# Performance work log

Measured on AMD Instinct MI355X. Metric: run time of the kernel, lower is better.

The kernel has to match this reference:

```python
import jax, jax.numpy as jnp
import numpy as np

ALPHA, BETA, GAMMA = 2.0, 2.0, 1.0
EPS = 1e-8  # torch F.cosine_similarity eps
B, T, D = 64, 1024, 256


def setup_inputs() -> dict:
    key = jax.random.key(0)
    k1, k2, k3 = jax.random.split(key, 3)
    f_v = jax.random.normal(k1, (B, T, D), dtype=jnp.float32)
    f_a = jax.random.normal(k2, (B, T, D), dtype=jnp.float32)
    labels = jax.random.randint(k3, (B,), 0, 2, dtype=jnp.int64)
    return {"f_v": f_v, "f_a": f_a, "labels": labels}


def _normalize(x):
    n = jnp.sqrt(jnp.sum(x * x, axis=-1, keepdims=True))
    return x / jnp.maximum(n, EPS)


def reference(f_v, f_a, labels):
    b, t, _ = f_v.shape
    vn = _normalize(f_v)  # [B,T,D]
    an = _normalize(f_a)  # [B,T,D]

    # --- per-timestep aligned-pair term ---
    cos_bt = jnp.sum(vn * an, axis=-1)  # [B,T] cosine sim
    d_bt = 1.0 - cos_bt                  # cosine distance
    pos_mask = (labels == 0).astype(f_v.dtype)[:, None]  # [B,1]
    neg_mask = 1.0 - pos_mask
    loss_pos = ALPHA * jnp.sum(d_bt * pos_mask)
    cnt_pos = jnp.sum(pos_mask) * t
    loss_neg = BETA * jnp.sum((1.0 - d_bt) * neg_mask)  # (1-d) == cos
    cnt_neg = jnp.sum(neg_mask) * t

    # --- cross-sample term: for i != j, (1 - mean_t d_ij) = mean_t cos(v_i_t, a_j_t) ---
    cross_cos = jnp.einsum('itd,jtd->ij', vn, an) / t  # [B,B] mean over T
    offdiag = 1.0 - jnp.eye(b, dtype=f_v.dtype)
    loss_neg = loss_neg + GAMMA * jnp.sum(cross_cos * offdiag)
    cnt_neg = cnt_neg + b * (b - 1)

    loss = jnp.where(cnt_pos > 0, loss_pos / jnp.maximum(cnt_pos, 1.0), 0.0)
    loss = loss + jnp.where(cnt_neg > 0, loss_neg / jnp.maximum(cnt_neg, 1.0), 0.0)
    return loss
```

## Files before the change

### kernel.cpp

```cpp
#include <hip/hip_runtime.h>

constexpr int Bn = 64;
constexpr int Tn = 1024;
constexpr int Dn = 256;

constexpr int TPB   = 256;
constexpr int RG    = 16;
constexpr int NG    = Bn / RG;
constexpr int PITCH = Dn + 4;

__device__ __forceinline__ float dot4(const float4& a, const float4& b) {
    return a.x * b.x + a.y * b.y + a.z * b.z + a.w * b.w;
}

__global__ __launch_bounds__(TPB, 4)
void cmfm_main(const float* __restrict__ fv, const float* __restrict__ fa,
               const int* __restrict__ labels, float* __restrict__ acc) {
    __shared__ __align__(16) float Vs[RG][PITCH];
    __shared__ __align__(16) float As[RG][PITCH];
    __shared__ float rvl[RG];
    __shared__ float ral[RG];
    __shared__ float wred[4][TPB / 64];

    const int tid = threadIdx.x;
    const int r16 = tid >> 4;
    const int dp  = tid & 15;
    const int t   = blockIdx.x;

    const float4* __restrict__ fv4 = reinterpret_cast<const float4*>(fv);
    const float4* __restrict__ fa4 = reinterpret_cast<const float4*>(fa);

    float pos_acc = 0.f, neg_acc = 0.f, diag_acc = 0.f;
    float svd = 0.f, sad = 0.f;

    for (int g = 0; g < NG; ++g) {
        const int row = g * RG + r16;
        const size_t base = ((size_t)row * Tn + t) * (Dn / 4);

        float4 v4[4], a4[4];
        #pragma unroll
        for (int k = 0; k < 4; ++k) {
            v4[k] = fv4[base + dp + 16 * k];
            a4[k] = fa4[base + dp + 16 * k];
        }
        float sqv = 0.f, sqa = 0.f, dva = 0.f;
        #pragma unroll
        for (int k = 0; k < 4; ++k) {
            sqv += dot4(v4[k], v4[k]);
            sqa += dot4(a4[k], a4[k]);
            dva += dot4(v4[k], a4[k]);
            const int d = (dp + 16 * k) * 4;
            *reinterpret_cast<float4*>(&Vs[r16][d]) = v4[k];
            *reinterpret_cast<float4*>(&As[r16][d]) = a4[k];
        }
        #pragma unroll
        for (int off = 1; off < 16; off <<= 1) {
            sqv += __shfl_xor(sqv, off);
            sqa += __shfl_xor(sqa, off);
            dva += __shfl_xor(dva, off);
        }
        if (dp == 0) {
            const float rv = 1.f / fmaxf(sqrtf(sqv), 1e-8f);
            const float ra = 1.f / fmaxf(sqrtf(sqa), 1e-8f);
            rvl[r16] = rv;
            ral[r16] = ra;
            const float cosd = dva * rv * ra;
            diag_acc += cosd;
            if (labels[row] == 0) pos_acc += 1.f - cosd;
            else                  neg_acc += cosd;
        }
        __syncthreads();

        #pragma unroll
        for (int i = 0; i < RG; ++i) {
            svd = fmaf(rvl[i], Vs[i][tid], svd);
            sad = fmaf(ral[i], As[i][tid], sad);
        }
        __syncthreads();
    }

    float dotp = svd * sad;
    #pragma unroll
    for (int off = 1; off < 64; off <<= 1) {
        pos_acc  += __shfl_xor(pos_acc, off);
        neg_acc  += __shfl_xor(neg_acc, off);
        diag_acc += __shfl_xor(diag_acc, off);
        dotp     += __shfl_xor(dotp, off);
    }
    const int wave = tid >> 6;
    const int lane = tid & 63;
    if (lane == 0) {
        wred[0][wave] = pos_acc;
        wred[1][wave] = neg_acc;
        wred[2][wave] = dotp;
        wred[3][wave] = diag_acc;
    }
    __syncthreads();
    if (tid == 0) {
        float p = 0.f, n = 0.f, o = 0.f, dg = 0.f;
        #pragma unroll
        for (int w = 0; w < TPB / 64; ++w) {
            p += wred[0][w]; n += wred[1][w]; o += wred[2][w]; dg += wred[3][w];
        }
        atomicAdd(&acc[0], p);
        atomicAdd(&acc[1], n);
        atomicAdd(&acc[2], o);
        atomicAdd(&acc[3], dg);
    }
}

__global__ void cmfm_final(const int* __restrict__ labels, const float* __restrict__ acc,
                           float* __restrict__ out) {
    if (threadIdx.x == 0) {
        int npos = 0;
        for (int i = 0; i < Bn; ++i) npos += (labels[i] == 0);
        const float pos_sum  = acc[0];
        const float neg_sum  = acc[1];
        const float dot_sum  = acc[2];
        const float diag_sum = acc[3];
        const float cross_sum = dot_sum - diag_sum;

        const float cnt_pos = (float)npos * (float)Tn;
        const float cnt_neg = (float)(Bn - npos) * (float)Tn + (float)Bn * (float)(Bn - 1);

        float loss = 0.f;
        if (npos > 0) loss += 2.0f * pos_sum / cnt_pos;
        loss += (2.0f * neg_sum + 1.0f * cross_sum / (float)Tn) / cnt_neg;
        out[0] = loss;
    }
}

extern "C" void kernel_launch(void* const* d_in, const int* in_sizes, int n_in,
                              void* d_out, int out_size, void* d_ws, size_t ws_size,
                              hipStream_t stream) {
    const float* fv     = (const float*)d_in[0];
    const float* fa     = (const float*)d_in[1];
    const int*   labels = (const int*)d_in[2];
    float* acc = (float*)d_ws;
    float* out = (float*)d_out;

    hipMemsetAsync(acc, 0, 4 * sizeof(float), stream);
    cmfm_main<<<Tn, TPB, 0, stream>>>(fv, fa, labels, acc);
    cmfm_final<<<1, 64, 0, stream>>>(labels, acc, out);
}
```

Measured before the change: 187.5 us.

## Split fused kernel into norms pass and cross-sum pass with workspace scales

The single fused kernel is split into two kernels. The first computes per-(sample, timestep) inverse norms and the diagonal cosine terms with many small blocks and writes the scales to workspace. The second rereads both inputs and accumulates the norm-scaled sums across samples, with no per-group syncthreads loop. This removes the serialized load/sync/LDS rounds and raises parallelism, at the cost of reading the 128 MB of input twice and adding a kernel launch.

```diff
diff --git a/kernel.cpp b/kernel.cpp
--- a/kernel.cpp
+++ b/kernel.cpp
@@ -1,112 +1,129 @@
 #include <hip/hip_runtime.h>
 
-constexpr int Bn = 64;
-constexpr int Tn = 1024;
-constexpr int Dn = 256;
-
-constexpr int TPB   = 256;
-constexpr int RG    = 16;
-constexpr int NG    = Bn / RG;
-constexpr int PITCH = Dn + 4;
+constexpr int Bn  = 64;
+constexpr int Tn  = 1024;
+constexpr int Dn  = 256;
+constexpr int TPB = 256;
 
 __device__ __forceinline__ float dot4(const float4& a, const float4& b) {
     return a.x * b.x + a.y * b.y + a.z * b.z + a.w * b.w;
 }
 
-__global__ __launch_bounds__(TPB, 4)
-void cmfm_main(const float* __restrict__ fv, const float* __restrict__ fa,
-               const int* __restrict__ labels, float* __restrict__ acc) {
-    __shared__ __align__(16) float Vs[RG][PITCH];
-    __shared__ __align__(16) float As[RG][PITCH];
-    __shared__ float rvl[RG];
-    __shared__ float ral[RG];
-    __shared__ float wred[4][TPB / 64];
+__global__ __launch_bounds__(TPB)
+void cmfm_norms(const float* __restrict__ fv, const float* __restrict__ fa,
+                const int* __restrict__ labels,
+                float* __restrict__ rv_ws, float* __restrict__ ra_ws,
+                float* __restrict__ acc) {
+    __shared__ float wred[3][4];
+    const int tid  = threadIdx.x;
+    const int lane = tid & 63;
+    const int wv   = tid >> 6;
+    const int i    = blockIdx.x >> 5;
+    const int tb   = blockIdx.x & 31;
+    const int tt   = lane >> 3;
+    const int d8   = lane & 7;
+    const int t    = tb * 32 + wv * 8 + tt;
 
-    const int tid = threadIdx.x;
-    const int r16 = tid >> 4;
-    const int dp  = tid & 15;
-    const int t   = blockIdx.x;
+    const float4* __restrict__ fv4 = reinterpret_cast<const float4*>(fv);
+    const float4* __restrict__ fa4 = reinterpret_cast<const float4*>(fa);
+    const size_t base = ((size_t)i * Tn + t) * (Dn / 4);
+
+    float4 v4[8], a4[8];
+    #pragma unroll
+    for (int k = 0; k < 8; ++k) v4[k] = fv4[base + d8 + 8 * k];
+    #pragma unroll
+    for (int k = 0; k < 8; ++k) a4[k] = fa4[base + d8 + 8 * k];
+
+    float sqv = 0.f, sqa = 0.f, dva = 0.f;
+    #pragma unroll
+    for (int k = 0; k < 8; ++k) {
+        sqv += dot4(v4[k], v4[k]);
+        sqa += dot4(a4[k], a4[k]);
+        dva += dot4(v4[k], a4[k]);
+    }
+    #pragma unroll
+    for (int off = 1; off < 8; off <<= 1) {
+        sqv += __shfl_xor(sqv, off);
+        sqa += __shfl_xor(sqa, off);
+        dva += __shfl_xor(dva, off);
+    }
+
+    float pos = 0.f, neg = 0.f, dg = 0.f;
+    const int lab = labels[i];
+    if (d8 == 0) {
+        const float rv = 1.f / fmaxf(sqrtf(sqv), 1e-8f);
+        const float ra = 1.f / fmaxf(sqrtf(sqa), 1e-8f);
+        rv_ws[t * Bn + i] = rv;
+        ra_ws[t * Bn + i] = ra;
+        const float cosd = dva * rv * ra;
+        dg = cosd;
+        if (lab == 0) pos = 1.f - cosd;
+        else          neg = cosd;
+    }
+    #pragma unroll
+    for (int off = 1; off < 64; off <<= 1) {
+        pos += __shfl_xor(pos, off);
+        neg += __shfl_xor(neg, off);
+        dg  += __shfl_xor(dg,  off);
+    }
+    if (lane == 0) { wred[0][wv] = pos; wred[1][wv] = neg; wred[2][wv] = dg; }
+    __syncthreads();
+    if (tid == 0) {
+        atomicAdd(&acc[0], wred[0][0] + wred[0][1] + wred[0][2] + wred[0][3]);
+        atomicAdd(&acc[1], wred[1][0] + wred[1][1] + wred[1][2] + wred[1][3]);
+        atomicAdd(&acc[3], wred[2][0] + wred[2][1] + wred[2][2] + wred[2][3]);
+    }
+}
+
+__global__ __launch_bounds__(TPB)
+void cmfm_cross(const float* __restrict__ fv, const float* __restrict__ fa,
+                const float* __restrict__ rv_ws, const float* __restrict__ ra_ws,
+                float* __restrict__ acc) {
+    __shared__ float rvsL[Bn];
+    __shared__ float rasL[Bn];
+    __shared__ __align__(16) float svL[4][Dn];
+    __shared__ __align__(16) float saL[4][Dn];
+    __shared__ float wred[4];
+
+    const int tid  = threadIdx.x;
+    const int lane = tid & 63;
+    const int wv   = tid >> 6;
+    const int t    = blockIdx.x;
+
+    if (tid < Bn)          rvsL[tid]      = rv_ws[t * Bn + tid];
+    else if (tid < 2 * Bn) rasL[tid - Bn] = ra_ws[t * Bn + tid - Bn];
+    __syncthreads();
 
     const float4* __restrict__ fv4 = reinterpret_cast<const float4*>(fv);
     const float4* __restrict__ fa4 = reinterpret_cast<const float4*>(fa);
 
-    float pos_acc = 0.f, neg_acc = 0.f, diag_acc = 0.f;
-    float svd = 0.f, sad = 0.f;
+    float4 sv = {0.f, 0.f, 0.f, 0.f}, sa = {0.f, 0.f, 0.f, 0.f};
+    const int i0 = wv * 16;
+    #pragma unroll
+    for (int k = 0; k < 16; ++k) {
+        const int i = i0 + k;
+        const size_t idx = ((size_t)i * Tn + t) * (Dn / 4) + lane;
+        const float4 v = fv4[idx];
+        const float4 a = fa4[idx];
+        const float rv = rvsL[i];
+        const float ra = rasL[i];
+        sv.x = fmaf(rv, v.x, sv.x); sv.y = fmaf(rv, v.y, sv.y);
+        sv.z = fmaf(rv, v.z, sv.z); sv.w = fmaf(rv, v.w, sv.w);
+        sa.x = fmaf(ra, a.x, sa.x); sa.y = fmaf(ra, a.y, sa.y);
+        sa.z = fmaf(ra, a.z, sa.z); sa.w = fmaf(ra, a.w, sa.w);
+    }
+    *reinterpret_cast<float4*>(&svL[wv][lane * 4]) = sv;
+    *reinterpret_cast<float4*>(&saL[wv][lane * 4]) = sa;
+    __syncthreads();
 
-    for (int g = 0; g < NG; ++g) {
-        const int row = g * RG + r16;
-        const size_t base = ((size_t)row * Tn + t) * (Dn / 4);
-
-        float4 v4[4], a4[4];
-        #pragma unroll
-        for (int k = 0; k < 4; ++k) {
-            v4[k] = fv4[base + dp + 16 * k];
-            a4[k] = fa4[base + dp + 16 * k];
-        }
-        float sqv = 0.f, sqa = 0.f, dva = 0.f;
-        #pragma unroll
-        for (int k = 0; k < 4; ++k) {
-            sqv += dot4(v4[k], v4[k]);
-            sqa += dot4(a4[k], a4[k]);
-            dva += dot4(v4[k], a4[k]);
-            const int d = (dp + 16 * k) * 4;
-            *reinterpret_cast<float4*>(&Vs[r16][d]) = v4[k];
-            *reinterpret_cast<float4*>(&As[r16][d]) = a4[k];
-        }
-        #pragma unroll
-        for (int off = 1; off < 16; off <<= 1) {
-            sqv += __shfl_xor(sqv, off);
-            sqa += __shfl_xor(sqa, off);
-            dva += __shfl_xor(dva, off);
-        }
-        if (dp == 0) {
-            const float rv = 1.f / fmaxf(sqrtf(sqv), 1e-8f);
-            const float ra = 1.f / fmaxf(sqrtf(sqa), 1e-8f);
-            rvl[r16] = rv;
-            ral[r16] = ra;
-            const float cosd = dva * rv * ra;
-            diag_acc += cosd;
-            if (labels[row] == 0) pos_acc += 1.f - cosd;
-            else                  neg_acc += cosd;
-        }
-        __syncthreads();
-
-        #pragma unroll
-        for (int i = 0; i < RG; ++i) {
-            svd = fmaf(rvl[i], Vs[i][tid], svd);
-            sad = fmaf(ral[i], As[i][tid], sad);
-        }
-        __syncthreads();
-    }
-
+    const float svd = svL[0][tid] + svL[1][tid] + svL[2][tid] + svL[3][tid];
+    const float sad = saL[0][tid] + saL[1][tid] + saL[2][tid] + saL[3][tid];
     float dotp = svd * sad;
     #pragma unroll
-    for (int off = 1; off < 64; off <<= 1) {
-        pos_acc  += __shfl_xor(pos_acc, off);
-        neg_acc  += __shfl_xor(neg_acc, off);
-        diag_acc += __shfl_xor(diag_acc, off);
-        dotp     += __shfl_xor(dotp, off);
-    }
-    const int wave = tid >> 6;
-    const int lane = tid & 63;
-    if (lane == 0) {
-        wred[0][wave] = pos_acc;
-        wred[1][wave] = neg_acc;
-        wred[2][wave] = dotp;
-        wred[3][wave] = diag_acc;
-    }
+    for (int off = 1; off < 64; off <<= 1) dotp += __shfl_xor(dotp, off);
+    if (lane == 0) wred[wv] = dotp;
     __syncthreads();
-    if (tid == 0) {
-        float p = 0.f, n = 0.f, o = 0.f, dg = 0.f;
-        #pragma unroll
-        for (int w = 0; w < TPB / 64; ++w) {
-            p += wred[0][w]; n += wred[1][w]; o += wred[2][w]; dg += wred[3][w];
-        }
-        atomicAdd(&acc[0], p);
-        atomicAdd(&acc[1], n);
-        atomicAdd(&acc[2], o);
-        atomicAdd(&acc[3], dg);
-    }
+    if (tid == 0) atomicAdd(&acc[2], wred[0] + wred[1] + wred[2] + wred[3]);
 }
 
 __global__ void cmfm_final(const int* __restrict__ labels, const float* __restrict__ acc,
@@ -136,10 +153,14 @@
     const float* fv     = (const float*)d_in[0];
     const float* fa     = (const float*)d_in[1];
     const int*   labels = (const int*)d_in[2];
-    float* acc = (float*)d_ws;
-    float* out = (float*)d_out;
+
+    float* rv_ws = (float*)d_ws;
+    float* ra_ws = rv_ws + (size_t)Tn * Bn;
+    float* acc   = ra_ws + (size_t)Tn * Bn;
+    float* out   = (float*)d_out;
 
     hipMemsetAsync(acc, 0, 4 * sizeof(float), stream);
-    cmfm_main<<<Tn, TPB, 0, stream>>>(fv, fa, labels, acc);
+    cmfm_norms<<<Bn * (Tn / 32), TPB, 0, stream>>>(fv, fa, labels, rv_ws, ra_ws, acc);
+    cmfm_cross<<<Tn, TPB, 0, stream>>>(fv, fa, rv_ws, ra_ws, acc);
     cmfm_final<<<1, 64, 0, stream>>>(labels, acc, out);
 }
```

After: 226.7 us. 1.21x slower.
